# Performance work log

Hardware: AMD Instinct MI355X
Metric: run time of the kernel (lower is better)

The kernel has to match this reference:

```python
import jax, jax.numpy as jnp
import numpy as np

DECAY = 0.99   # LIF membrane decay
INH = 1.625    # lateral inhibition strength (mode='max')


def setup_inputs() -> dict:
    key = jax.random.key(0)
    kx, kw = jax.random.split(key)
    B, Cin, Cout = 8192, 4096, 1024
    x = (jax.random.uniform(kx, (B, Cin)) < 0.2).astype(jnp.float32)
    # weights, then normweight(): clamp to [0,1] and scale each row so row-max == 0.1
    W = jax.random.uniform(kw, (Cout, Cin), dtype=jnp.float32)
    W = W / (W.max(axis=1, keepdims=True) / 0.1)
    return {"x": x, "W": W, "time_window": 10}


def reference(x, W, time_window):
    # current through the bias-free linear layer; constant across timesteps
    i = x @ W.T                                   # (B, Cout)
    # adaptive threshold init: threshold = 3 * max over batch (thre_init branch)
    thr = 3.0 * i.max(axis=0)                     # (Cout,)
    imax = i.max(axis=1, keepdims=True)           # (B, 1), for mode='max' inhibition
    C = i.shape[1]

    def step(mem, _):
        mem = mem * DECAY + i                     # LIF integration
        s = (mem > thr).astype(i.dtype)           # threshold fire
        mem = mem * (1.0 - s)                     # hard reset at all spikers
        row = s.max(axis=1, keepdims=True)        # (B,1) 1 if any neuron in row spiked
        # winner-take-all k=1: keep a single spiking neuron per row (first/argmax)
        wta = jax.nn.one_hot(jnp.argmax(s, axis=1), C, dtype=i.dtype) * row
        # lateral inhibition: subtract inh * max-current from losers in rows that spiked
        mem = mem - INH * imax * (row - wta)
        return mem, wta

    mem0 = jnp.zeros_like(i)
    _, wtas = jax.lax.scan(step, mem0, None, length=time_window)
    return wtas.sum(axis=0)                       # accumulated spikes (B, Cout)
```

## Files before the change

### kernel.cpp

```cpp
#include <hip/hip_runtime.h>
#include <cstdint>

#define B_DIM 8192
#define CIN   4096
#define COUT  1024

constexpr double W_SCALE   = 83230720.0;
constexpr int    QMAX      = 8323072;
constexpr double INV_SCALE = 0.1 / 8323072.0;

using i32x4 = __attribute__((ext_vector_type(4))) int;

__device__ __forceinline__ void async_copy16(void* lds, const void* g) {
    auto l = (__attribute__((address_space(3))) void*)(uintptr_t)(lds);
    auto p = (const __attribute__((address_space(1))) void*)(uintptr_t)(g);
    __builtin_amdgcn_global_load_lds(p, l, 16, 0, 0);
}

__global__ void prep_xw(const float* __restrict__ x, const float* __restrict__ W,
                        int8_t* __restrict__ Ai, int8_t* __restrict__ Bd,
                        unsigned long long* __restrict__ cm) {
    const int bid = blockIdx.x;
    if (bid < 8192) {
        const int idx = bid * 256 + threadIdx.x;
        const float4* xp = (const float4*)x + (size_t)idx * 4;
        float4 v0 = xp[0], v1 = xp[1], v2 = xp[2], v3 = xp[3];
        auto pk = [](float a, float b, float c, float d) -> int {
            return (a != 0.f ? 1 : 0) | ((b != 0.f ? 1 : 0) << 8) |
                   ((c != 0.f ? 1 : 0) << 16) | ((d != 0.f ? 1 : 0) << 24);
        };
        int4 r;
        r.x = pk(v0.x, v0.y, v0.z, v0.w);
        r.y = pk(v1.x, v1.y, v1.z, v1.w);
        r.z = pk(v2.x, v2.y, v2.z, v2.w);
        r.w = pk(v3.x, v3.y, v3.z, v3.w);
        ((int4*)Ai)[idx] = r;
    } else {
        const int idx = (bid - 8192) * 256 + threadIdx.x;
        float4 w = ((const float4*)W)[idx];
        float ws[4] = {w.x, w.y, w.z, w.w};
        char dg[3][4];
#pragma unroll
        for (int k = 0; k < 4; ++k) {
            int qv = __double2int_rn((double)ws[k] * W_SCALE);
            qv = max(0, min(QMAX, qv));
            int d0 = ((qv + 128) & 255) - 128; int tq = (qv - d0) >> 8;
            int d1 = ((tq + 128) & 255) - 128; int d2 = (tq - d1) >> 8;
            dg[0][k] = (char)d0; dg[1][k] = (char)d1; dg[2][k] = (char)d2;
        }
        const size_t off = (size_t)idx * 4;
#pragma unroll
        for (int p = 0; p < 3; ++p) {
            char4 c4; c4.x = dg[p][0]; c4.y = dg[p][1]; c4.z = dg[p][2]; c4.w = dg[p][3];
            *(char4*)(Bd + (size_t)p * COUT * CIN + off) = c4;
        }
        if (idx < COUT) cm[idx] = 0ull;
    }
}

__device__ __forceinline__ void mma16(const i32x4 (&a)[8], const i32x4 (&b)[4],
                                      i32x4 (*accp)[2]) {
    __builtin_amdgcn_s_setprio(1);
#pragma unroll
    for (int kk = 0; kk < 2; ++kk)
#pragma unroll
        for (int mi = 0; mi < 4; ++mi)
#pragma unroll
            for (int ni = 0; ni < 2; ++ni)
                accp[mi][ni] = __builtin_amdgcn_mfma_i32_16x16x64_i8(
                    a[kk * 4 + mi], b[kk * 2 + ni], accp[mi][ni], 0, 0, 0);
    __builtin_amdgcn_s_setprio(0);
}

#define BAR()    __builtin_amdgcn_s_barrier()
#define SCHED0() __builtin_amdgcn_sched_barrier(0)
#define VMW(n)   asm volatile("s_waitcnt vmcnt(" #n ")" ::: "memory")

__global__ __launch_bounds__(256, 2) void gemm_i8(const int8_t* __restrict__ A,
                                                  const int8_t* __restrict__ Bm,
                                                  double* __restrict__ Sc,
                                                  unsigned long long* __restrict__ cm) {
    __shared__ alignas(16) int8_t lds[65536];
    const int tid  = threadIdx.x;
    const int lane = tid & 63;
    const int wave = tid >> 6;

    const int wg = (int)blockIdx.x;
    const int bn = ((wg & 7) << 1) | ((wg >> 3) & 1);
    const int bm = wg >> 4;

    const int stid   = tid >> 3;
    const int cswz16 = ((tid & 7) ^ (stid & 7)) << 4;
    const int8_t* gA = A  + (size_t)(bm * 128 + stid) * CIN + cswz16;
    const int8_t* gB = Bm + (size_t)(bn * 64  + stid) * CIN + cswz16;
    const int wv1024 = wave << 10;

#define SA_(t_) do {                                                            \
    int8_t* d_ = lds + wv1024;                                                  \
    const int8_t* s_ = gA + ((t_) << 7);                                        \
    async_copy16(d_,         s_);                                               \
    async_copy16(d_ + 4096,  s_ + (size_t)32 * CIN);                            \
    async_copy16(d_ + 8192,  s_ + (size_t)64 * CIN);                            \
    async_copy16(d_ + 12288, s_ + (size_t)96 * CIN);                            \
} while (0)
#define SB_(t_, p_, db_) do {                                                   \
    int8_t* d_ = lds + 16384 + ((p_) << 14) + ((db_) << 13) + wv1024;           \
    const int8_t* s_ = gB + (size_t)(p_) * COUT * CIN + ((t_) << 7);            \
    async_copy16(d_,        s_);                                                \
    async_copy16(d_ + 4096, s_ + (size_t)32 * CIN);                             \
} while (0)

    const int wr = wave >> 1, wc = wave & 1;
    const int fr = lane & 15;
    const int q  = lane >> 4;
    const int ck0 = (q ^ (fr & 7)) << 4;
    const int abase = (wr * 64 + fr) * 128;
    const int bbase = (wc * 32 + fr) * 128;

    i32x4 a[8], bX[4], bY[4];
    i32x4 acc[3][4][2] = {};

#define LDA_() do {                                                             \
    const int8_t* p_ = lds + abase;                                             \
    _Pragma("unroll")                                                           \
    for (int kk_ = 0; kk_ < 2; ++kk_)                                           \
        _Pragma("unroll")                                                       \
        for (int mi_ = 0; mi_ < 4; ++mi_)                                       \
            a[kk_ * 4 + mi_] = *(const i32x4*)(p_ + mi_ * 2048 + (ck0 ^ (kk_ * 64))); \
} while (0)
#define LDB_(dst_, p_, db_) do {                                                \
    const int8_t* q_ = lds + 16384 + ((p_) << 14) + ((db_) << 13) + bbase;      \
    _Pragma("unroll")                                                           \
    for (int kk_ = 0; kk_ < 2; ++kk_)                                           \
        _Pragma("unroll")                                                       \
        for (int ni_ = 0; ni_ < 2; ++ni_)                                       \
            dst_[kk_ * 2 + ni_] = *(const i32x4*)(q_ + ni_ * 2048 + (ck0 ^ (kk_ * 64))); \
} while (0)

#define TILE(t_, dR_, dW_, b0_, b1_)                                            \
     LDA_(); LDB_(b1_, 1, dR_); SB_((t_) + 1, 0, dW_);                  \
    SCHED0(); mma16(a, b0_, acc[0]); VMW(2); BAR(); SCHED0();                   \
     LDB_(b0_, 2, dR_); SA_((t_) + 1); SB_((t_) + 1, 1, dW_);           \
    SCHED0(); mma16(a, b1_, acc[1]); VMW(6); BAR(); SCHED0();                   \
     LDB_(b1_, 0, dW_); SB_((t_) + 1, 2, dW_);                          \
    SCHED0(); mma16(a, b0_, acc[2]); VMW(2); BAR(); SCHED0();

    SA_(0); SB_(0, 0, 0); SB_(0, 1, 0); SB_(0, 2, 0);
    VMW(2); BAR(); SCHED0();
    LDB_(bX, 0, 0);

#pragma unroll 1
    for (int t = 0; t < 30; t += 2) {
        TILE(t,     0, 1, bX, bY)
        TILE(t + 1, 1, 0, bY, bX)
    }
    TILE(30, 0, 1, bX, bY)
    LDA_(); LDB_(bX, 1, 1);
    SCHED0(); mma16(a, bY, acc[0]); VMW(0); BAR(); SCHED0();
    LDB_(bY, 2, 1);
    SCHED0(); mma16(a, bX, acc[1]); BAR(); SCHED0();
    SCHED0(); mma16(a, bY, acc[2]); BAR();

    const int gm0 = bm * 128 + wr * 64 + q * 4;
    const int gn0 = bn * 64 + wc * 32 + fr;
    double vmax[2] = {0.0, 0.0};
#pragma unroll
    for (int mi = 0; mi < 4; ++mi)
#pragma unroll
        for (int ni = 0; ni < 2; ++ni) {
            const int gn = gn0 + ni * 16;
#pragma unroll
            for (int reg = 0; reg < 4; ++reg) {
                const int gm = gm0 + mi * 16 + reg;
                long long isum = (long long)acc[0][mi][ni][reg]
                               + 256ll   * (long long)acc[1][mi][ni][reg]
                               + 65536ll * (long long)acc[2][mi][ni][reg];
                double v = (double)isum * INV_SCALE;
                Sc[(size_t)gm * COUT + gn] = v;
                vmax[ni] = fmax(vmax[ni], v);
            }
        }
#pragma unroll
    for (int ni = 0; ni < 2; ++ni) {
        vmax[ni] = fmax(vmax[ni], __shfl_xor(vmax[ni], 16, 64));
        vmax[ni] = fmax(vmax[ni], __shfl_xor(vmax[ni], 32, 64));
    }
    double* red = (double*)lds;
    if (lane < 16) {
#pragma unroll
        for (int ni = 0; ni < 2; ++ni)
            red[wave * 32 + ni * 16 + fr] = vmax[ni];
    }
    __syncthreads();
    if (tid < 64) {
        const int c = tid;
        double m = fmax(red[c], red[64 + c]);
        atomicMax(cm + bn * 64 + c, (unsigned long long)__double_as_longlong(m));
    }
#undef SA_
#undef SB_
#undef LDA_
#undef LDB_
#undef TILE
}

__global__ void scan_k(const double* __restrict__ Sc, const unsigned long long* __restrict__ cm,
                       const int* __restrict__ twp, float* __restrict__ out) {
    const int lane = threadIdx.x & 63;
    const int wave = threadIdx.x >> 6;
    const int b = blockIdx.x * 4 + wave;
    const int T = *twp;
    const double* row = Sc + (size_t)b * COUT;

    double iv[16], mem[16], thr[16];
    int cnt[16];
    double imax = 0.0;
#pragma unroll
    for (int u = 0; u < 16; ++u) {
        const int j = lane + u * 64;
        iv[u]  = row[j];
        thr[u] = 3.0 * __longlong_as_double((long long)cm[j]);
        mem[u] = 0.0; cnt[u] = 0;
        imax = fmax(imax, iv[u]);
    }
#pragma unroll
    for (int d = 32; d >= 1; d >>= 1) imax = fmax(imax, __shfl_xor(imax, d, 64));
    const double h = 1.625 * imax;

    for (int t = 0; t < T; ++t) {
        int first = 0x7fffffff;
        bool sp[16];
#pragma unroll
        for (int u = 0; u < 16; ++u) {
            mem[u] = mem[u] * 0.99 + iv[u];
            sp[u] = mem[u] > thr[u];
            if (sp[u]) first = min(first, lane + u * 64);
        }
#pragma unroll
        for (int d = 32; d >= 1; d >>= 1) first = min(first, __shfl_xor(first, d, 64));
        const bool rowspike = first < 0x7fffffff;
#pragma unroll
        for (int u = 0; u < 16; ++u) {
            if (sp[u]) mem[u] = 0.0;
            if (rowspike) {
                if (lane + u * 64 == first) cnt[u]++;
                else mem[u] -= h;
            }
        }
    }
#pragma unroll
    for (int u = 0; u < 16; ++u)
        out[(size_t)b * COUT + lane + u * 64] = (float)cnt[u];
}

extern "C" void kernel_launch(void* const* d_in, const int* in_sizes, int n_in,
                              void* d_out, int out_size, void* d_ws, size_t ws_size,
                              hipStream_t stream) {
    const float* x  = (const float*)d_in[0];
    const float* W  = (const float*)d_in[1];
    const int*   tw = (const int*)d_in[2];
    float* out = (float*)d_out;

    int8_t* Ai = (int8_t*)d_ws;
    int8_t* Bd = Ai + (size_t)B_DIM * CIN;
    double* Sc = (double*)(Bd + (size_t)3 * COUT * CIN);
    unsigned long long* cm =
        (unsigned long long*)((int8_t*)Sc + (size_t)B_DIM * COUT * 8);

    hipLaunchKernelGGL(prep_xw, dim3(12288), dim3(256), 0, stream, x, W, Ai, Bd, cm);
    hipLaunchKernelGGL(gemm_i8, dim3(1024),  dim3(256), 0, stream, Ai, Bd, Sc, cm);
    hipLaunchKernelGGL(scan_k,  dim3(2048),  dim3(256), 0, stream, Sc, cm, tw, out);
}
```

Baseline: 325.5 us.

## Double-buffer full A/B tiles in GEMM and store currents as float32

Replaces the hand-interleaved three-phase staggered B-plane pipeline with a simple whole-tile double buffer: each iteration issues async loads for the next k-tile of A and all three B digit planes, then reads every fragment and runs all MFMAs, followed by one wait and barrier. LDS grows to 80 KB per block. Separately, the intermediate current matrix and the column-max buffer shrink from double to float, halving the GEMM-to-scan traffic. The float rounding could change threshold comparisons in the scan, and the larger LDS footprint may reduce how many blocks fit per CU.

New measurement: 323.2 us, median of 2. About the same (-0.7%).

```diff
diff --git a/kernel.cpp b/kernel.cpp
--- a/kernel.cpp
+++ b/kernel.cpp
@@ -19,7 +19,7 @@
 
 __global__ void prep_xw(const float* __restrict__ x, const float* __restrict__ W,
                         int8_t* __restrict__ Ai, int8_t* __restrict__ Bd,
-                        unsigned long long* __restrict__ cm) {
+                        unsigned int* __restrict__ cm) {
     const int bid = blockIdx.x;
     if (bid < 8192) {
         const int idx = bid * 256 + threadIdx.x;
@@ -54,22 +54,8 @@
             char4 c4; c4.x = dg[p][0]; c4.y = dg[p][1]; c4.z = dg[p][2]; c4.w = dg[p][3];
             *(char4*)(Bd + (size_t)p * COUT * CIN + off) = c4;
         }
-        if (idx < COUT) cm[idx] = 0ull;
-    }
-}
-
-__device__ __forceinline__ void mma16(const i32x4 (&a)[8], const i32x4 (&b)[4],
-                                      i32x4 (*accp)[2]) {
-    __builtin_amdgcn_s_setprio(1);
-#pragma unroll
-    for (int kk = 0; kk < 2; ++kk)
-#pragma unroll
-        for (int mi = 0; mi < 4; ++mi)
-#pragma unroll
-            for (int ni = 0; ni < 2; ++ni)
-                accp[mi][ni] = __builtin_amdgcn_mfma_i32_16x16x64_i8(
-                    a[kk * 4 + mi], b[kk * 2 + ni], accp[mi][ni], 0, 0, 0);
-    __builtin_amdgcn_s_setprio(0);
+        if (idx < COUT) cm[idx] = 0u;
+    }
 }
 
 #define BAR()    __builtin_amdgcn_s_barrier()
@@ -78,9 +64,9 @@
 
 __global__ __launch_bounds__(256, 2) void gemm_i8(const int8_t* __restrict__ A,
                                                   const int8_t* __restrict__ Bm,
-                                                  double* __restrict__ Sc,
-                                                  unsigned long long* __restrict__ cm) {
-    __shared__ alignas(16) int8_t lds[65536];
+                                                  float* __restrict__ Sc,
+                                                  unsigned int* __restrict__ cm) {
+    __shared__ alignas(16) int8_t lds[81920];
     const int tid  = threadIdx.x;
     const int lane = tid & 63;
     const int wave = tid >> 6;
@@ -95,75 +81,85 @@
     const int8_t* gB = Bm + (size_t)(bn * 64  + stid) * CIN + cswz16;
     const int wv1024 = wave << 10;
 
-#define SA_(t_) do {                                                            \
-    int8_t* d_ = lds + wv1024;                                                  \
+#define SA_(t_, d_) do {                                                        \
+    int8_t* d2_ = lds + ((d_) << 14) + wv1024;                                  \
     const int8_t* s_ = gA + ((t_) << 7);                                        \
-    async_copy16(d_,         s_);                                               \
-    async_copy16(d_ + 4096,  s_ + (size_t)32 * CIN);                            \
-    async_copy16(d_ + 8192,  s_ + (size_t)64 * CIN);                            \
-    async_copy16(d_ + 12288, s_ + (size_t)96 * CIN);                            \
-} while (0)
-#define SB_(t_, p_, db_) do {                                                   \
-    int8_t* d_ = lds + 16384 + ((p_) << 14) + ((db_) << 13) + wv1024;           \
+    async_copy16(d2_,         s_);                                              \
+    async_copy16(d2_ + 4096,  s_ + (size_t)32 * CIN);                           \
+    async_copy16(d2_ + 8192,  s_ + (size_t)64 * CIN);                           \
+    async_copy16(d2_ + 12288, s_ + (size_t)96 * CIN);                           \
+} while (0)
+#define SB_(t_, p_, d_) do {                                                    \
+    int8_t* d2_ = lds + 32768 + ((p_) << 14) + ((d_) << 13) + wv1024;           \
     const int8_t* s_ = gB + (size_t)(p_) * COUT * CIN + ((t_) << 7);            \
-    async_copy16(d_,        s_);                                                \
-    async_copy16(d_ + 4096, s_ + (size_t)32 * CIN);                             \
+    async_copy16(d2_,        s_);                                               \
+    async_copy16(d2_ + 4096, s_ + (size_t)32 * CIN);                            \
 } while (0)
 
     const int wr = wave >> 1, wc = wave & 1;
     const int fr = lane & 15;
     const int q  = lane >> 4;
     const int ck0 = (q ^ (fr & 7)) << 4;
+    const int ck1 = ck0 ^ 64;
     const int abase = (wr * 64 + fr) * 128;
     const int bbase = (wc * 32 + fr) * 128;
 
-    i32x4 a[8], bX[4], bY[4];
+    i32x4 a[8], b0[4], b1[4], b2[4];
     i32x4 acc[3][4][2] = {};
 
-#define LDA_() do {                                                             \
-    const int8_t* p_ = lds + abase;                                             \
+#define M8(accp_, ao_, bv_, bo_) do {                                           \
+    __builtin_amdgcn_s_setprio(1);                                              \
     _Pragma("unroll")                                                           \
-    for (int kk_ = 0; kk_ < 2; ++kk_)                                           \
-        _Pragma("unroll")                                                       \
-        for (int mi_ = 0; mi_ < 4; ++mi_)                                       \
-            a[kk_ * 4 + mi_] = *(const i32x4*)(p_ + mi_ * 2048 + (ck0 ^ (kk_ * 64))); \
-} while (0)
-#define LDB_(dst_, p_, db_) do {                                                \
-    const int8_t* q_ = lds + 16384 + ((p_) << 14) + ((db_) << 13) + bbase;      \
-    _Pragma("unroll")                                                           \
-    for (int kk_ = 0; kk_ < 2; ++kk_)                                           \
+    for (int mi_ = 0; mi_ < 4; ++mi_)                                           \
         _Pragma("unroll")                                                       \
         for (int ni_ = 0; ni_ < 2; ++ni_)                                       \
-            dst_[kk_ * 2 + ni_] = *(const i32x4*)(q_ + ni_ * 2048 + (ck0 ^ (kk_ * 64))); \
-} while (0)
-
-#define TILE(t_, dR_, dW_, b0_, b1_)                                            \
-     LDA_(); LDB_(b1_, 1, dR_); SB_((t_) + 1, 0, dW_);                  \
-    SCHED0(); mma16(a, b0_, acc[0]); VMW(2); BAR(); SCHED0();                   \
-     LDB_(b0_, 2, dR_); SA_((t_) + 1); SB_((t_) + 1, 1, dW_);           \
-    SCHED0(); mma16(a, b1_, acc[1]); VMW(6); BAR(); SCHED0();                   \
-     LDB_(b1_, 0, dW_); SB_((t_) + 1, 2, dW_);                          \
-    SCHED0(); mma16(a, b0_, acc[2]); VMW(2); BAR(); SCHED0();
-
-    SA_(0); SB_(0, 0, 0); SB_(0, 1, 0); SB_(0, 2, 0);
-    VMW(2); BAR(); SCHED0();
-    LDB_(bX, 0, 0);
+            accp_[mi_][ni_] = __builtin_amdgcn_mfma_i32_16x16x64_i8(            \
+                a[(ao_) + mi_], bv_[(bo_) + ni_], accp_[mi_][ni_], 0, 0, 0);    \
+    __builtin_amdgcn_s_setprio(0);                                              \
+} while (0)
+
+#define READS_(pr_) do {                                                        \
+    const int8_t* ap_  = lds + ((pr_) << 14) + abase;                           \
+    const int8_t* bp0_ = lds + 32768 +         ((pr_) << 13) + bbase;           \
+    const int8_t* bp1_ = lds + 32768 + 16384 + ((pr_) << 13) + bbase;           \
+    const int8_t* bp2_ = lds + 32768 + 32768 + ((pr_) << 13) + bbase;           \
+                                    \
+    a[0] = *(const i32x4*)(ap_ + ck0);         a[1] = *(const i32x4*)(ap_ + 2048 + ck0); \
+    a[2] = *(const i32x4*)(ap_ + 4096 + ck0);  a[3] = *(const i32x4*)(ap_ + 6144 + ck0); \
+    b0[0] = *(const i32x4*)(bp0_ + ck0);       b0[1] = *(const i32x4*)(bp0_ + 2048 + ck0); \
+    b1[0] = *(const i32x4*)(bp1_ + ck0);       b1[1] = *(const i32x4*)(bp1_ + 2048 + ck0); \
+    b2[0] = *(const i32x4*)(bp2_ + ck0);       b2[1] = *(const i32x4*)(bp2_ + 2048 + ck0); \
+                                          \
+    a[4] = *(const i32x4*)(ap_ + ck1);         a[5] = *(const i32x4*)(ap_ + 2048 + ck1); \
+    a[6] = *(const i32x4*)(ap_ + 4096 + ck1);  a[7] = *(const i32x4*)(ap_ + 6144 + ck1); \
+    b0[2] = *(const i32x4*)(bp0_ + ck1);       b0[3] = *(const i32x4*)(bp0_ + 2048 + ck1); \
+    b1[2] = *(const i32x4*)(bp1_ + ck1);       b1[3] = *(const i32x4*)(bp1_ + 2048 + ck1); \
+    b2[2] = *(const i32x4*)(bp2_ + ck1);       b2[3] = *(const i32x4*)(bp2_ + 2048 + ck1); \
+} while (0)
+
+#define MMAS_() do {                                                            \
+    M8(acc[0], 0, b0, 0); M8(acc[1], 0, b1, 0); M8(acc[2], 0, b2, 0);           \
+    M8(acc[0], 4, b0, 2); M8(acc[1], 4, b1, 2); M8(acc[2], 4, b2, 2);           \
+} while (0)
+
+    SA_(0, 0); SB_(0, 0, 0); SB_(0, 1, 0); SB_(0, 2, 0);
+    VMW(0); BAR();
 
 #pragma unroll 1
-    for (int t = 0; t < 30; t += 2) {
-        TILE(t,     0, 1, bX, bY)
-        TILE(t + 1, 1, 0, bY, bX)
-    }
-    TILE(30, 0, 1, bX, bY)
-    LDA_(); LDB_(bX, 1, 1);
-    SCHED0(); mma16(a, bY, acc[0]); VMW(0); BAR(); SCHED0();
-    LDB_(bY, 2, 1);
-    SCHED0(); mma16(a, bX, acc[1]); BAR(); SCHED0();
-    SCHED0(); mma16(a, bY, acc[2]); BAR();
+    for (int t = 0; t < 31; ++t) {
+        const int pr = t & 1, pw = pr ^ 1;
+        SA_(t + 1, pw); SB_(t + 1, 0, pw); SB_(t + 1, 1, pw); SB_(t + 1, 2, pw);
+        SCHED0();
+        READS_(pr);
+        MMAS_();
+        SCHED0(); VMW(0); BAR();
+    }
+    READS_(1);
+    MMAS_();
 
     const int gm0 = bm * 128 + wr * 64 + q * 4;
     const int gn0 = bn * 64 + wc * 32 + fr;
-    double vmax[2] = {0.0, 0.0};
+    float vmax[2] = {0.f, 0.f};
 #pragma unroll
     for (int mi = 0; mi < 4; ++mi)
 #pragma unroll
@@ -175,17 +171,17 @@
                 long long isum = (long long)acc[0][mi][ni][reg]
                                + 256ll   * (long long)acc[1][mi][ni][reg]
                                + 65536ll * (long long)acc[2][mi][ni][reg];
-                double v = (double)isum * INV_SCALE;
+                float v = (float)((double)isum * INV_SCALE);
                 Sc[(size_t)gm * COUT + gn] = v;
-                vmax[ni] = fmax(vmax[ni], v);
+                vmax[ni] = fmaxf(vmax[ni], v);
             }
         }
 #pragma unroll
     for (int ni = 0; ni < 2; ++ni) {
-        vmax[ni] = fmax(vmax[ni], __shfl_xor(vmax[ni], 16, 64));
-        vmax[ni] = fmax(vmax[ni], __shfl_xor(vmax[ni], 32, 64));
-    }
-    double* red = (double*)lds;
+        vmax[ni] = fmaxf(vmax[ni], __shfl_xor(vmax[ni], 16, 64));
+        vmax[ni] = fmaxf(vmax[ni], __shfl_xor(vmax[ni], 32, 64));
+    }
+    float* red = (float*)lds;
     if (lane < 16) {
 #pragma unroll
         for (int ni = 0; ni < 2; ++ni)
@@ -194,23 +190,23 @@
     __syncthreads();
     if (tid < 64) {
         const int c = tid;
-        double m = fmax(red[c], red[64 + c]);
-        atomicMax(cm + bn * 64 + c, (unsigned long long)__double_as_longlong(m));
+        float m = fmaxf(red[c], red[64 + c]);
+        atomicMax(cm + bn * 64 + c, __float_as_uint(m));
     }
 #undef SA_
 #undef SB_
-#undef LDA_
-#undef LDB_
-#undef TILE
-}
-
-__global__ void scan_k(const double* __restrict__ Sc, const unsigned long long* __restrict__ cm,
+#undef M8
+#undef READS_
+#undef MMAS_
+}
+
+__global__ void scan_k(const float* __restrict__ Sc, const unsigned int* __restrict__ cm,
                        const int* __restrict__ twp, float* __restrict__ out) {
     const int lane = threadIdx.x & 63;
     const int wave = threadIdx.x >> 6;
     const int b = blockIdx.x * 4 + wave;
     const int T = *twp;
-    const double* row = Sc + (size_t)b * COUT;
+    const float* row = Sc + (size_t)b * COUT;
 
     double iv[16], mem[16], thr[16];
     int cnt[16];
@@ -218,8 +214,8 @@
 #pragma unroll
     for (int u = 0; u < 16; ++u) {
         const int j = lane + u * 64;
-        iv[u]  = row[j];
-        thr[u] = 3.0 * __longlong_as_double((long long)cm[j]);
+        iv[u]  = (double)row[j];
+        thr[u] = 3.0 * (double)__uint_as_float(cm[j]);
         mem[u] = 0.0; cnt[u] = 0;
         imax = fmax(imax, iv[u]);
     }
@@ -263,9 +259,9 @@
 
     int8_t* Ai = (int8_t*)d_ws;
     int8_t* Bd = Ai + (size_t)B_DIM * CIN;
-    double* Sc = (double*)(Bd + (size_t)3 * COUT * CIN);
-    unsigned long long* cm =
-        (unsigned long long*)((int8_t*)Sc + (size_t)B_DIM * COUT * 8);
+    float*  Sc = (float*)(Bd + (size_t)3 * COUT * CIN);
+    unsigned int* cm =
+        (unsigned int*)((int8_t*)Sc + (size_t)B_DIM * COUT * 4);
 
     hipLaunchKernelGGL(prep_xw, dim3(12288), dim3(256), 0, stream, x, W, Ai, Bd, cm);
     hipLaunchKernelGGL(gemm_i8, dim3(1024),  dim3(256), 0, stream, Ai, Bd, Sc, cm);
```
